# Optimization experiments

Measured on AMD Instinct MI355X. Metric: run time of the kernel, lower is better.

## Reference

```python
import jax, jax.numpy as jnp
import numpy as np

TINY = 1e-9
S, V, H, W = 2, 4, 1024, 1024
PATCH, SKIP = 2, 2
C = PATCH * SKIP
PIX_PER_VIEW = 4096
NP_COARSE = PIX_PER_VIEW // (PATCH * PATCH)   # top-k on coarse grid
N_SAMPLED = NP_COARSE * PATCH * PATCH         # total fine pixels per view
ON_MASK = 0.9
AT_CENTER = 0.8
HC, WC = H // C, W // C


def setup_inputs() -> dict:
    key = jax.random.key(0)
    k1, k2, k3, k4, k5 = jax.random.split(key, 5)
    ys, xs = jnp.meshgrid(jnp.arange(H, dtype=jnp.float32),
                          jnp.arange(W, dtype=jnp.float32), indexing='ij')
    uv1 = jnp.stack([xs.reshape(-1), ys.reshape(-1)])            # (2, H*W): X then Y
    uv = jnp.broadcast_to(uv1[None, None], (S, V, 2, H * W)) + 0.0
    base = jnp.array([[1111.0, 0.0, W / 2.0, 0.0],
                      [0.0, 1111.0, H / 2.0, 0.0],
                      [0.0, 0.0, 1.0, 0.0],
                      [0.0, 0.0, 0.0, 1.0]], dtype=jnp.float32)
    intrinsics = jnp.broadcast_to(base[None], (S, 4, 4)) + 0.0
    A = jax.random.normal(k2, (S, V, 3, 3), dtype=jnp.float32)
    Q, _ = jnp.linalg.qr(A)                                       # random rotations
    t = 2.0 * jax.random.normal(k3, (S, V, 3), dtype=jnp.float32)
    ext = jnp.zeros((S, V, 4, 4), dtype=jnp.float32)
    ext = ext.at[..., :3, :3].set(Q).at[..., :3, 3].set(t).at[..., 3, 3].set(1.0)
    alpha = jax.random.normal(k4, (S, V, H, W), dtype=jnp.float32)
    size = jnp.stack([jnp.full((S, V), H, jnp.int32),
                      jnp.full((S, V), W, jnp.int32)], axis=-1)
    gumbel_u = jax.random.uniform(k5, (S, V, HC * WC), dtype=jnp.float32)
    full_index = jax.random.randint(k1, (S, V), 0, SKIP * SKIP)
    return dict(uv=uv, intrinsics=intrinsics, extrinsics=ext, alpha=alpha,
                size=size, gumbel_u=gumbel_u, full_index=full_index)


def _sample_pixels(uv, alpha, gumbel_u, full_index):
    # mask from alpha, restricted to image center (sampling_at_center=0.8)
    mask = (alpha > 0).astype(jnp.float32)                        # (S,V,H,W)
    r = (1.0 - AT_CENTER) / 2.0
    rh, rw = int(H * r), int(W * r)
    row_ok = (jnp.arange(H) >= rh) & (jnp.arange(H) < H - rh)
    col_ok = (jnp.arange(W) >= rw) & (jnp.arange(W) < W - rw)
    mask = mask * (row_ok[:, None] & col_ok[None, :]).astype(jnp.float32)
    probs = mask / (mask.sum() + 1e-8)                            # global normalization as in torch
    probs = ON_MASK * probs + (1.0 - ON_MASK) / (H * W)
    # pool probabilities onto the coarse (patch*skip) grid
    probs_c = probs.reshape(S, V, HC, C, WC, C).sum(axis=(3, 5))  # (S,V,HC,WC)
    logp = jnp.log(probs_c.reshape(S, V, -1) + TINY)
    g = -jnp.log(-jnp.log(gumbel_u + TINY) + TINY)                # gumbel noise
    idx = jax.lax.top_k(logp + g, NP_COARSE)[1]                   # (S,V,NP_COARSE)
    sm = jnp.zeros((S, V, HC * WC), jnp.float32)
    sm = sm.at[jnp.arange(S)[:, None, None], jnp.arange(V)[None, :, None], idx].set(1.0)
    sm = sm.reshape(S, V, HC, WC)
    # expand each coarse cell into a patch x patch block -> (S,V,H//SKIP,W//SKIP)
    sm = jnp.broadcast_to(sm[:, :, :, None, :, None],
                          (S, V, HC, PATCH, WC, PATCH)).reshape(S, V, H // SKIP, W // SKIP)
    # scatter into a random skip-slot per view, then interleave skip grid
    oh = jax.nn.one_hot(full_index, SKIP * SKIP, dtype=jnp.float32)  # (S,V,SKIP*SKIP)
    full = oh[:, :, :, None, None] * sm[:, :, None, :, :]
    sm = full.reshape(S, V, SKIP, SKIP, H // SKIP, W // SKIP)
    sm = sm.transpose(0, 1, 4, 2, 5, 3).reshape(S, V, H, W)
    # row-major gather of sampled pixels (matches torch boolean-mask gather)
    mflat = sm.reshape(S, V, H * W)
    order = jnp.argsort(-mflat, axis=-1)[..., :N_SAMPLED]         # stable: ones in row-major order
    Xs = jnp.take_along_axis(uv[:, :, 0], order, axis=-1).reshape(S, V, 1, -1, PATCH, PATCH)
    Ys = jnp.take_along_axis(uv[:, :, 1], order, axis=-1).reshape(S, V, 1, -1, PATCH, PATCH)
    return jnp.concatenate([Xs, Ys], axis=2)                      # (S,V,2,NPatch,PATCH,PATCH)


def _rays(uv_s, intrinsics, extrinsics):
    fuv = uv_s.reshape(S, V, 2, -1)                               # (S,V,2,N)
    ray_start = extrinsics[:, :, :3, 3]                           # (S,V,3)
    fx = intrinsics[:, 0, 0][:, None, None]
    fy = intrinsics[:, 1, 1][:, None, None]
    cx = intrinsics[:, 0, 2][:, None, None]
    cy = intrinsics[:, 1, 2][:, None, None]
    x = (fuv[:, :, 0] - cx) / fx                                  # z = 1 lift
    y = (fuv[:, :, 1] - cy) / fy
    ones = jnp.ones_like(x)
    cam = jnp.stack([x, y, ones, ones], axis=2)                   # (S,V,4,N) homogeneous
    world = jnp.einsum('svij,svjn->svin', extrinsics, cam)[:, :, :3]
    d = world - ray_start[..., None]
    d = d / jnp.maximum(jnp.linalg.norm(d, axis=2, keepdims=True), 1e-12)
    return ray_start[:, :, None, :], d.transpose(0, 1, 3, 2)      # (S,V,1,3), (S,V,N,3)


def reference(uv, intrinsics, extrinsics, alpha, size, gumbel_u, full_index):
    uv_s = _sample_pixels(uv, alpha, gumbel_u, full_index)
    ray_start, ray_dir = _rays(uv_s, intrinsics, extrinsics)
    return ray_start, ray_dir, uv_s
```

## Files before the change

kernel.cpp:

```cpp
#include <hip/hip_runtime.h>
#include <math.h>

#define S_ 2
#define V_ 4
#define H_ 1024
#define W_ 1024
#define NCELL 65536
#define NSV 8
#define KSEL 1024
#define CROP_LO 102
#define CROP_HI 922

#define NB1 32768
#define NB2 131072
#define HIST_U4 ((NB1 + NB2) * NSV / 4)

#define OFF_SEL   64
#define OFF_SEG1  256
#define OFF_SEG2  4352
#define OFF_CNT   8448
#define OFF_ROW   8448
#define OFF_KEYS  532736
#define OFF_H1    2629888
#define OFF_H2    3678464

static __device__ __forceinline__ unsigned score_key(float score){
  unsigned ub = __float_as_uint(score);
  return (ub & 0x80000000u) ? ~ub : (ub | 0x80000000u);
}

__global__ __launch_bounds__(1024) void k_init(unsigned* __restrict__ ws32){
  int t = threadIdx.x;
  if (t == 0) ws32[0] = 0u;
  ws32[64 + t] = 0u;
  ws32[64 + 1024 + t] = 0u;
}

__global__ __launch_bounds__(256) void k_count(const float* __restrict__ alpha,
                                               unsigned char* __restrict__ cnt,
                                               unsigned* __restrict__ total){
  int g = blockIdx.x * 256 + threadIdx.x;
  int sv = g >> 16;
  int cell = g & (NCELL - 1);
  int hc = cell >> 8;
  int wc = cell & 255;
  const float4* ap = reinterpret_cast<const float4*>(alpha);
  int c = 0;
  int x0 = wc * 4;
#pragma unroll
  for (int dy = 0; dy < 4; ++dy){
    int y = hc * 4 + dy;
    float4 a = ap[(size_t)(sv * H_ + y) * (W_ / 4) + wc];
    if (y >= CROP_LO && y < CROP_HI){
      c += (a.x > 0.0f) & (x0 + 0 >= CROP_LO) & (x0 + 0 < CROP_HI);
      c += (a.y > 0.0f) & (x0 + 1 >= CROP_LO) & (x0 + 1 < CROP_HI);
      c += (a.z > 0.0f) & (x0 + 2 >= CROP_LO) & (x0 + 2 < CROP_HI);
      c += (a.w > 0.0f) & (x0 + 3 >= CROP_LO) & (x0 + 3 < CROP_HI);
    }
  }
  cnt[g] = (unsigned char)c;
  __shared__ unsigned red[256];
  red[threadIdx.x] = (unsigned)c;
  __syncthreads();
  for (int off = 128; off > 0; off >>= 1){
    if (threadIdx.x < off) red[threadIdx.x] += red[threadIdx.x + off];
    __syncthreads();
  }
  if (threadIdx.x == 0) atomicAdd(total, red[0]);
}

__global__ __launch_bounds__(256) void k_score(const unsigned char* __restrict__ cnt,
                                               const float* __restrict__ gum,
                                               const unsigned* __restrict__ total,
                                               unsigned* __restrict__ keys,
                                               uint4* __restrict__ histz){
  int g = blockIdx.x * 256 + threadIdx.x;
  if (g < HIST_U4) histz[g] = make_uint4(0u, 0u, 0u, 0u);
  float T = (float)(*total);
  float denom = __fadd_rn(T, 1e-8f);
  float inv = __fdiv_rn(1.0f, denom);
  const float COFF = (float)((1.0 - 0.9) / (1024.0 * 1024.0));
  float q_on = __fadd_rn(__fmul_rn(0.9f, inv), COFF);
  int k = cnt[g];
  float pc = __fadd_rn(__fmul_rn((float)k, q_on), __fmul_rn((float)(16 - k), COFF));
  float logp = logf(__fadd_rn(pc, 1e-9f));
  float u = gum[g];
  float gl = logf(__fadd_rn(u, 1e-9f));
  float gmb = -logf(__fadd_rn(-gl, 1e-9f));
  keys[g] = score_key(__fadd_rn(logp, gmb));
}

__global__ __launch_bounds__(256) void k_hist1(const unsigned* __restrict__ keys,
                                               unsigned* __restrict__ hist1,
                                               unsigned* __restrict__ segsum1){
  int sv = blockIdx.x >> 5;
  int chunk = blockIdx.x & 31;
  __shared__ unsigned h[NB1 / 2];
  for (int i = threadIdx.x; i < NB1 / 2; i += 256) h[i] = 0u;
  __syncthreads();
  const uint4* kp = reinterpret_cast<const uint4*>(keys + sv * NCELL + chunk * 2048);
#pragma unroll
  for (int i = 0; i < 2; ++i){
    uint4 k4 = kp[threadIdx.x + i * 256];
    unsigned b;
    b = k4.x >> 17; atomicAdd(&h[b >> 1], 1u << ((b & 1u) << 4));
    b = k4.y >> 17; atomicAdd(&h[b >> 1], 1u << ((b & 1u) << 4));
    b = k4.z >> 17; atomicAdd(&h[b >> 1], 1u << ((b & 1u) << 4));
    b = k4.w >> 17; atomicAdd(&h[b >> 1], 1u << ((b & 1u) << 4));
  }
  __syncthreads();
  unsigned* hb = hist1 + sv * NB1;
  for (int i = threadIdx.x; i < NB1 / 2; i += 256){
    unsigned w = h[i];
    unsigned lo = w & 0xFFFFu, hi = w >> 16;
    if (lo) atomicAdd(&hb[2 * i + 0], lo);
    if (hi) atomicAdd(&hb[2 * i + 1], hi);
  }
  if (threadIdx.x < 128){
    unsigned s = 0;
    for (int i = 0; i < 128; ++i){
      unsigned w = h[threadIdx.x * 128 + i];
      s += (w & 0xFFFFu) + (w >> 16);
    }
    if (s) atomicAdd(&segsum1[sv * 128 + threadIdx.x], s);
  }
}

__global__ __launch_bounds__(256) void k_pick1b(const unsigned* __restrict__ hist1,
                                                const unsigned* __restrict__ segsum1,
                                                unsigned* __restrict__ sel){
  const int sv = blockIdx.x;
  const int t = threadIdx.x;
  __shared__ unsigned ss[128];
  __shared__ int swin;
  __shared__ unsigned stgt;
  __shared__ unsigned sh[256];
  if (t < 128) ss[t] = segsum1[sv * 128 + t];
  __syncthreads();
  if (t == 0){
    unsigned target = KSEL, cum = 0;
    for (int s = 127; s >= 0; --s){
      cum += ss[s];
      if (cum >= target){ swin = s; stgt = target - (cum - ss[s]); break; }
    }
  }
  __syncthreads();
  unsigned v = hist1[sv * NB1 + swin * 256 + t];
  sh[t] = v;
  __syncthreads();
  for (int off = 1; off < 256; off <<= 1){
    unsigned y = (t + off < 256) ? sh[t + off] : 0u;
    __syncthreads();
    sh[t] += y;
    __syncthreads();
  }
  unsigned sufAbove = sh[t] - v;
  if (sufAbove < stgt && sh[t] >= stgt){
    sel[sv * 4 + 0] = (unsigned)(swin * 256 + t);
    sel[sv * 4 + 1] = stgt - sufAbove;
  }
}

__global__ __launch_bounds__(256) void k_hist2(const unsigned* __restrict__ keys,
                                               const unsigned* __restrict__ sel,
                                               unsigned* __restrict__ hist2,
                                               unsigned* __restrict__ segsum2){
  int sv = blockIdx.x >> 5;
  int chunk = blockIdx.x & 31;
  unsigned p15 = sel[sv * 4 + 0];
  __shared__ unsigned seg[128];
  if (threadIdx.x < 128) seg[threadIdx.x] = 0u;
  __syncthreads();
  const uint4* kp = reinterpret_cast<const uint4*>(keys + sv * NCELL + chunk * 2048);
  unsigned* hb = hist2 + sv * NB2;
#pragma unroll
  for (int i = 0; i < 2; ++i){
    uint4 k4 = kp[threadIdx.x + i * 256];
    unsigned kk[4] = {k4.x, k4.y, k4.z, k4.w};
#pragma unroll
    for (int q = 0; q < 4; ++q){
      if ((kk[q] >> 17) == p15){
        unsigned low = kk[q] & 0x1FFFFu;
        atomicAdd(&hb[low], 1u);
        atomicAdd(&seg[low >> 10], 1u);
      }
    }
  }
  __syncthreads();
  if (threadIdx.x < 128){
    unsigned s = seg[threadIdx.x];
    if (s) atomicAdd(&segsum2[sv * 128 + threadIdx.x], s);
  }
}

__global__ __launch_bounds__(256) void k_pick2c(const unsigned* __restrict__ hist2,
                                                const unsigned* __restrict__ segsum2,
                                                unsigned* __restrict__ sel){
  const int sv = blockIdx.x;
  const int t = threadIdx.x;
  __shared__ unsigned ss[128];
  __shared__ int swin;
  __shared__ unsigned stgt;
  __shared__ unsigned sh[256];
  if (t < 128) ss[t] = segsum2[sv * 128 + t];
  __syncthreads();
  if (t == 0){
    unsigned target = sel[sv * 4 + 1];
    unsigned cum = 0;
    for (int s = 127; s >= 0; --s){
      cum += ss[s];
      if (cum >= target){ swin = s; stgt = target - (cum - ss[s]); break; }
    }
  }
  __syncthreads();
  const int s = swin;
  const unsigned t2 = stgt;
  uint4 v = reinterpret_cast<const uint4*>(hist2 + sv * NB2 + s * 1024)[t];
  unsigned csum = v.x + v.y + v.z + v.w;
  sh[t] = csum;
  __syncthreads();
  for (int off = 1; off < 256; off <<= 1){
    unsigned y = (t + off < 256) ? sh[t + off] : 0u;
    __syncthreads();
    sh[t] += y;
    __syncthreads();
  }
  unsigned sufAbove = sh[t] - csum;
  if (sufAbove < t2 && sh[t] >= t2){
    unsigned bb[4] = {v.x, v.y, v.z, v.w};
    unsigned cum = sufAbove;
    for (int b = 3; b >= 0; --b){
      cum += bb[b];
      if (cum >= t2){
        sel[sv * 4 + 2] = (sel[sv * 4 + 0] << 17) | (unsigned)(s * 1024 + t * 4 + b);
        sel[sv * 4 + 3] = t2 - (cum - bb[b]);
        break;
      }
    }
  }
}

__global__ __launch_bounds__(256) void k_rowcnt(const unsigned* __restrict__ keys,
                                                const unsigned* __restrict__ sel,
                                                unsigned* __restrict__ rowcnt){
  int gw = blockIdx.x * 4 + (threadIdx.x >> 6);
  int lane = threadIdx.x & 63;
  int sv = gw >> 8;
  int row = gw & 255;
  const unsigned thr = sel[sv * 4 + 2];
  uint4 k4 = *reinterpret_cast<const uint4*>(keys + sv * NCELL + row * 256 + lane * 4);
  unsigned gt = (k4.x > thr) + (k4.y > thr) + (k4.z > thr) + (k4.w > thr);
  unsigned eq = (k4.x == thr) + (k4.y == thr) + (k4.z == thr) + (k4.w == thr);
  unsigned p = (gt << 16) | eq;
#pragma unroll
  for (int off = 1; off < 64; off <<= 1) p += __shfl_xor(p, off, 64);
  if (lane == 0) rowcnt[gw] = p;
}

static __device__ __forceinline__ unsigned block_excl_scan256(unsigned v, unsigned* lds4, int t){
  int lane = t & 63, w = t >> 6;
  unsigned x = v;
#pragma unroll
  for (int off = 1; off < 64; off <<= 1){
    unsigned y = __shfl_up(x, (unsigned)off, 64);
    if (lane >= off) x += y;
  }
  if (lane == 63) lds4[w] = x;
  __syncthreads();
  unsigned base = 0;
  for (int i = 0; i < w; ++i) base += lds4[i];
  __syncthreads();
  return base + x - v;
}

__global__ __launch_bounds__(256) void k_emitray(const unsigned* __restrict__ keys,
                                                 const unsigned* __restrict__ sel,
                                                 const unsigned* __restrict__ rowcnt,
                                                 const int* __restrict__ fidx,
                                                 const float* __restrict__ intr,
                                                 const float* __restrict__ extr,
                                                 float* __restrict__ out){
  const int sv = blockIdx.x >> 6;
  const int t = threadIdx.x;
  __shared__ unsigned lds4[4];
  __shared__ unsigned sM[256], sP[256], sEqb[256];

  const unsigned thr = sel[sv * 4 + 2];
  const unsigned rem = sel[sv * 4 + 3];

  unsigned rc = rowcnt[sv * 256 + t];
  unsigned gt = rc >> 16, eq = rc & 0xFFFFu;
  unsigned eqbase = block_excl_scan256(eq, lds4, t);
  unsigned take_eq = 0;
  if (rem > eqbase){ take_eq = rem - eqbase; if (take_eq > eq) take_eq = eq; }
  unsigned m = gt + take_eq;
  unsigned P = block_excl_scan256(m, lds4, t);
  sM[t] = m; sP[t] = P; sEqb[t] = eqbase;
  __syncthreads();

  const int lane = t & 63;
  const int row = ((blockIdx.x & 63) << 2) + (t >> 6);
  const unsigned rm = sM[row];
  const unsigned rP = sP[row];
  const unsigned reqb = sEqb[row];

  const int s = sv >> 2;
  const float fx = intr[s * 16 + 0];
  const float cx = intr[s * 16 + 2];
  const float fy = intr[s * 16 + 5];
  const float cy = intr[s * 16 + 6];
  const float e00 = extr[sv * 16 + 0], e01 = extr[sv * 16 + 1], e02 = extr[sv * 16 + 2], e03 = extr[sv * 16 + 3];
  const float e10 = extr[sv * 16 + 4], e11 = extr[sv * 16 + 5], e12 = extr[sv * 16 + 6], e13 = extr[sv * 16 + 7];
  const float e20 = extr[sv * 16 + 8], e21 = extr[sv * 16 + 9], e22 = extr[sv * 16 + 10], e23 = extr[sv * 16 + 11];
  if ((blockIdx.x & 63) == 0 && t < 3) out[sv * 3 + t] = extr[sv * 16 + t * 4 + 3];

  const int fi = fidx[sv];
  const int k1 = (fi >> 1) & 1;
  const int k2 = fi & 1;
  float* out_dir = out + S_ * V_ * 3;
  float* out_uvs = out + S_ * V_ * 3 + S_ * V_ * 4096 * 3;

  uint4 k4 = *reinterpret_cast<const uint4*>(keys + sv * NCELL + row * 256 + lane * 4);
  unsigned kk[4] = {k4.x, k4.y, k4.z, k4.w};

  unsigned laneEq = 0;
#pragma unroll
  for (int q = 0; q < 4; ++q) laneEq += (kk[q] == thr);
  unsigned xe = laneEq;
#pragma unroll
  for (int off = 1; off < 64; off <<= 1){
    unsigned y = __shfl_up(xe, (unsigned)off, 64);
    if (lane >= off) xe += y;
  }
  unsigned eqpre = xe - laneEq;

  bool ssel[4];
  unsigned eqr = reqb + eqpre;
  unsigned laneSel = 0;
#pragma unroll
  for (int q = 0; q < 4; ++q){
    bool sq = (kk[q] > thr);
    if (kk[q] == thr){ if (eqr < rem) sq = true; eqr++; }
    ssel[q] = sq;
    laneSel += sq;
  }
  unsigned xs = laneSel;
#pragma unroll
  for (int off = 1; off < 64; off <<= 1){
    unsigned y = __shfl_up(xs, (unsigned)off, 64);
    if (lane >= off) xs += y;
  }
  unsigned jj = xs - laneSel;

  const unsigned baserank = 4u * rP;
#pragma unroll
  for (int q = 0; q < 4; ++q){
    if (!ssel[q]) continue;
    int wc = lane * 4 + q;
    unsigned base = baserank + 2u * jj;
    int y0 = 4 * row + k1;
    int x0 = 4 * wc + k2;
#pragma unroll
    for (int p1 = 0; p1 < 2; ++p1){
#pragma unroll
      for (int p2 = 0; p2 < 2; ++p2){
        unsigned r = base + (unsigned)p1 * 2u * rm + (unsigned)p2;
        float X = (float)(x0 + 2 * p2);
        float Y = (float)(y0 + 2 * p1);
        out_uvs[(sv * 2 + 0) * 4096 + r] = X;
        out_uvs[(sv * 2 + 1) * 4096 + r] = Y;
        float xx = (X - cx) / fx;
        float yy = (Y - cy) / fy;
        float d0 = (e00 * xx + e01 * yy + e02 + e03) - e03;
        float d1 = (e10 * xx + e11 * yy + e12 + e13) - e13;
        float d2 = (e20 * xx + e21 * yy + e22 + e23) - e23;
        float nrm = sqrtf(d0 * d0 + d1 * d1 + d2 * d2);
        float den = fmaxf(nrm, 1e-12f);
        size_t ob = ((size_t)sv * 4096 + r) * 3;
        out_dir[ob + 0] = d0 / den;
        out_dir[ob + 1] = d1 / den;
        out_dir[ob + 2] = d2 / den;
      }
    }
    jj++;
  }
}

extern "C" void kernel_launch(void* const* d_in, const int* in_sizes, int n_in,
                              void* d_out, int out_size, void* d_ws, size_t ws_size,
                              hipStream_t stream){
  (void)in_sizes; (void)n_in; (void)out_size; (void)ws_size;
  const float* intr       = (const float*)d_in[1];
  const float* extr       = (const float*)d_in[2];
  const float* alpha      = (const float*)d_in[3];
  const float* gum        = (const float*)d_in[5];
  const int*   full_index = (const int*)d_in[6];
  float* out = (float*)d_out;

  char* ws = (char*)d_ws;
  unsigned*      ws32    = (unsigned*)ws;
  unsigned*      total   = (unsigned*)ws;
  unsigned*      sel     = (unsigned*)(ws + OFF_SEL);
  unsigned*      segsum1 = (unsigned*)(ws + OFF_SEG1);
  unsigned*      segsum2 = (unsigned*)(ws + OFF_SEG2);
  unsigned char* cnt     = (unsigned char*)(ws + OFF_CNT);
  unsigned*      rowcnt  = (unsigned*)(ws + OFF_ROW);
  unsigned*      keys    = (unsigned*)(ws + OFF_KEYS);
  unsigned*      hist1   = (unsigned*)(ws + OFF_H1);
  unsigned*      hist2   = (unsigned*)(ws + OFF_H2);
  uint4*         histz   = (uint4*)(ws + OFF_H1);

  hipLaunchKernelGGL(k_init,    dim3(1), dim3(1024), 0, stream, ws32);
  hipLaunchKernelGGL(k_count,   dim3(NSV * NCELL / 256), dim3(256), 0, stream, alpha, cnt, total);
  hipLaunchKernelGGL(k_score,   dim3(NSV * NCELL / 256), dim3(256), 0, stream, cnt, gum, total, keys, histz);
  hipLaunchKernelGGL(k_hist1,   dim3(NSV * 32), dim3(256), 0, stream, keys, hist1, segsum1);
  hipLaunchKernelGGL(k_pick1b,  dim3(NSV), dim3(256), 0, stream, hist1, segsum1, sel);
  hipLaunchKernelGGL(k_hist2,   dim3(NSV * 32), dim3(256), 0, stream, keys, sel, hist2, segsum2);
  hipLaunchKernelGGL(k_pick2c,  dim3(NSV), dim3(256), 0, stream, hist2, segsum2, sel);
  hipLaunchKernelGGL(k_rowcnt,  dim3(512), dim3(256), 0, stream, keys, sel, rowcnt);
  hipLaunchKernelGGL(k_emitray, dim3(512), dim3(256), 0, stream, keys, sel, rowcnt, full_index, intr, extr, out);
}
```

Baseline: 82.48 us.

## Fuse score, histogram and pick stages using last-block completion counters

Removes the init kernel and folds workspace zeroing into the count kernel. The global atomic total becomes per-block partial sums that each scoring block reduces itself. Scoring is fused with the first radix histogram, and each pick step now runs in the last block to finish (detected with done counters and threadfences), so the launch count drops from nine to five. In exchange every scoring block re-reduces 2048 partials, and the pick work now runs serially inside a single tail block.

```diff
diff --git a/kernel.cpp b/kernel.cpp
--- a/kernel.cpp
+++ b/kernel.cpp
@@ -16,30 +16,30 @@
 #define HIST_U4 ((NB1 + NB2) * NSV / 4)
 
 #define OFF_SEL   64
+#define OFF_DONE  192
 #define OFF_SEG1  256
 #define OFF_SEG2  4352
-#define OFF_CNT   8448
-#define OFF_ROW   8448
-#define OFF_KEYS  532736
-#define OFF_H1    2629888
-#define OFF_H2    3678464
+#define OFF_PART  8448
+#define OFF_CNT   16640
+#define OFF_ROW   16640
+#define OFF_KEYS  540928
+#define OFF_H1    2638080
+#define OFF_H2    3686656
 
 static __device__ __forceinline__ unsigned score_key(float score){
   unsigned ub = __float_as_uint(score);
   return (ub & 0x80000000u) ? ~ub : (ub | 0x80000000u);
 }
 
-__global__ __launch_bounds__(1024) void k_init(unsigned* __restrict__ ws32){
-  int t = threadIdx.x;
-  if (t == 0) ws32[0] = 0u;
-  ws32[64 + t] = 0u;
-  ws32[64 + 1024 + t] = 0u;
-}
-
 __global__ __launch_bounds__(256) void k_count(const float* __restrict__ alpha,
                                                unsigned char* __restrict__ cnt,
-                                               unsigned* __restrict__ total){
+                                               unsigned* __restrict__ partial,
+                                               uint4* __restrict__ histz,
+                                               unsigned* __restrict__ ws32){
   int g = blockIdx.x * 256 + threadIdx.x;
+  if (g < HIST_U4) histz[g] = make_uint4(0u, 0u, 0u, 0u);
+  if (g < 2048) ws32[64 + g] = 0u;
+  if (g < 16)   ws32[48 + g] = 0u;
   int sv = g >> 16;
   int cell = g & (NCELL - 1);
   int hc = cell >> 8;
@@ -66,116 +66,138 @@
     if (threadIdx.x < off) red[threadIdx.x] += red[threadIdx.x + off];
     __syncthreads();
   }
-  if (threadIdx.x == 0) atomicAdd(total, red[0]);
-}
-
-__global__ __launch_bounds__(256) void k_score(const unsigned char* __restrict__ cnt,
-                                               const float* __restrict__ gum,
-                                               const unsigned* __restrict__ total,
-                                               unsigned* __restrict__ keys,
-                                               uint4* __restrict__ histz){
-  int g = blockIdx.x * 256 + threadIdx.x;
-  if (g < HIST_U4) histz[g] = make_uint4(0u, 0u, 0u, 0u);
-  float T = (float)(*total);
+  if (threadIdx.x == 0) partial[blockIdx.x] = red[0];
+}
+
+__global__ __launch_bounds__(256) void k_scoreh(const unsigned char* __restrict__ cnt,
+                                                const float* __restrict__ gum,
+                                                const unsigned* __restrict__ partial,
+                                                unsigned* __restrict__ keys,
+                                                unsigned* __restrict__ hist1,
+                                                unsigned* __restrict__ segsum1,
+                                                unsigned* __restrict__ done1,
+                                                unsigned* __restrict__ sel){
+  const int sv = blockIdx.x >> 5;
+  const int chunk = blockIdx.x & 31;
+  const int t = threadIdx.x;
+  __shared__ unsigned h[NB1 / 2];
+  __shared__ unsigned red[256];
+  __shared__ unsigned ss[128];
+  __shared__ unsigned sh2[256];
+  __shared__ int swin;
+  __shared__ unsigned stgt;
+  __shared__ int slast;
+
+  unsigned psum = 0;
+#pragma unroll
+  for (int j = 0; j < 8; ++j) psum += partial[t + j * 256];
+  red[t] = psum;
+  __syncthreads();
+  for (int off = 128; off > 0; off >>= 1){
+    if (t < off) red[t] += red[t + off];
+    __syncthreads();
+  }
+  const float T = (float)red[0];
+
   float denom = __fadd_rn(T, 1e-8f);
   float inv = __fdiv_rn(1.0f, denom);
   const float COFF = (float)((1.0 - 0.9) / (1024.0 * 1024.0));
   float q_on = __fadd_rn(__fmul_rn(0.9f, inv), COFF);
-  int k = cnt[g];
-  float pc = __fadd_rn(__fmul_rn((float)k, q_on), __fmul_rn((float)(16 - k), COFF));
-  float logp = logf(__fadd_rn(pc, 1e-9f));
-  float u = gum[g];
-  float gl = logf(__fadd_rn(u, 1e-9f));
-  float gmb = -logf(__fadd_rn(-gl, 1e-9f));
-  keys[g] = score_key(__fadd_rn(logp, gmb));
-}
-
-__global__ __launch_bounds__(256) void k_hist1(const unsigned* __restrict__ keys,
-                                               unsigned* __restrict__ hist1,
-                                               unsigned* __restrict__ segsum1){
-  int sv = blockIdx.x >> 5;
-  int chunk = blockIdx.x & 31;
-  __shared__ unsigned h[NB1 / 2];
-  for (int i = threadIdx.x; i < NB1 / 2; i += 256) h[i] = 0u;
-  __syncthreads();
-  const uint4* kp = reinterpret_cast<const uint4*>(keys + sv * NCELL + chunk * 2048);
-#pragma unroll
-  for (int i = 0; i < 2; ++i){
-    uint4 k4 = kp[threadIdx.x + i * 256];
-    unsigned b;
-    b = k4.x >> 17; atomicAdd(&h[b >> 1], 1u << ((b & 1u) << 4));
-    b = k4.y >> 17; atomicAdd(&h[b >> 1], 1u << ((b & 1u) << 4));
-    b = k4.z >> 17; atomicAdd(&h[b >> 1], 1u << ((b & 1u) << 4));
-    b = k4.w >> 17; atomicAdd(&h[b >> 1], 1u << ((b & 1u) << 4));
+
+  unsigned kreg[8];
+  const int base = sv * NCELL + chunk * 2048;
+#pragma unroll
+  for (int i = 0; i < 8; ++i){
+    int g = base + i * 256 + t;
+    int k = cnt[g];
+    float pc = __fadd_rn(__fmul_rn((float)k, q_on), __fmul_rn((float)(16 - k), COFF));
+    float logp = logf(__fadd_rn(pc, 1e-9f));
+    float u = gum[g];
+    float gl = logf(__fadd_rn(u, 1e-9f));
+    float gmb = -logf(__fadd_rn(-gl, 1e-9f));
+    kreg[i] = score_key(__fadd_rn(logp, gmb));
+    keys[g] = kreg[i];
+  }
+
+  for (int i = t; i < NB1 / 2; i += 256) h[i] = 0u;
+  __syncthreads();
+#pragma unroll
+  for (int i = 0; i < 8; ++i){
+    unsigned b = kreg[i] >> 17;
+    atomicAdd(&h[b >> 1], 1u << ((b & 1u) << 4));
   }
   __syncthreads();
   unsigned* hb = hist1 + sv * NB1;
-  for (int i = threadIdx.x; i < NB1 / 2; i += 256){
+  for (int i = t; i < NB1 / 2; i += 256){
     unsigned w = h[i];
     unsigned lo = w & 0xFFFFu, hi = w >> 16;
     if (lo) atomicAdd(&hb[2 * i + 0], lo);
     if (hi) atomicAdd(&hb[2 * i + 1], hi);
   }
-  if (threadIdx.x < 128){
+  if (t < 128){
     unsigned s = 0;
     for (int i = 0; i < 128; ++i){
-      unsigned w = h[threadIdx.x * 128 + i];
+      unsigned w = h[t * 128 + i];
       s += (w & 0xFFFFu) + (w >> 16);
     }
-    if (s) atomicAdd(&segsum1[sv * 128 + threadIdx.x], s);
-  }
-}
-
-__global__ __launch_bounds__(256) void k_pick1b(const unsigned* __restrict__ hist1,
-                                                const unsigned* __restrict__ segsum1,
-                                                unsigned* __restrict__ sel){
-  const int sv = blockIdx.x;
+    if (s) atomicAdd(&segsum1[sv * 128 + t], s);
+  }
+
+  __threadfence();
+  if (t == 0) slast = (atomicAdd(&done1[sv], 1u) == 31u) ? 1 : 0;
+  __syncthreads();
+  if (slast){
+    __threadfence();
+    if (t < 128) ss[t] = segsum1[sv * 128 + t];
+    __syncthreads();
+    if (t == 0){
+      unsigned target = KSEL, cum = 0;
+      for (int s = 127; s >= 0; --s){
+        cum += ss[s];
+        if (cum >= target){ swin = s; stgt = target - (cum - ss[s]); break; }
+      }
+    }
+    __syncthreads();
+    unsigned v = hist1[sv * NB1 + swin * 256 + t];
+    sh2[t] = v;
+    __syncthreads();
+    for (int off = 1; off < 256; off <<= 1){
+      unsigned y = (t + off < 256) ? sh2[t + off] : 0u;
+      __syncthreads();
+      sh2[t] += y;
+      __syncthreads();
+    }
+    unsigned sufAbove = sh2[t] - v;
+    if (sufAbove < stgt && sh2[t] >= stgt){
+      sel[sv * 4 + 0] = (unsigned)(swin * 256 + t);
+      sel[sv * 4 + 1] = stgt - sufAbove;
+    }
+  }
+}
+
+__global__ __launch_bounds__(256) void k_hist2p(const unsigned* __restrict__ keys,
+                                                unsigned* __restrict__ sel,
+                                                unsigned* __restrict__ hist2,
+                                                unsigned* __restrict__ segsum2,
+                                                unsigned* __restrict__ done2){
+  const int sv = blockIdx.x >> 5;
+  const int chunk = blockIdx.x & 31;
   const int t = threadIdx.x;
+  __shared__ unsigned seg[128];
   __shared__ unsigned ss[128];
+  __shared__ unsigned sh2[256];
   __shared__ int swin;
   __shared__ unsigned stgt;
-  __shared__ unsigned sh[256];
-  if (t < 128) ss[t] = segsum1[sv * 128 + t];
-  __syncthreads();
-  if (t == 0){
-    unsigned target = KSEL, cum = 0;
-    for (int s = 127; s >= 0; --s){
-      cum += ss[s];
-      if (cum >= target){ swin = s; stgt = target - (cum - ss[s]); break; }
-    }
-  }
-  __syncthreads();
-  unsigned v = hist1[sv * NB1 + swin * 256 + t];
-  sh[t] = v;
-  __syncthreads();
-  for (int off = 1; off < 256; off <<= 1){
-    unsigned y = (t + off < 256) ? sh[t + off] : 0u;
-    __syncthreads();
-    sh[t] += y;
-    __syncthreads();
-  }
-  unsigned sufAbove = sh[t] - v;
-  if (sufAbove < stgt && sh[t] >= stgt){
-    sel[sv * 4 + 0] = (unsigned)(swin * 256 + t);
-    sel[sv * 4 + 1] = stgt - sufAbove;
-  }
-}
-
-__global__ __launch_bounds__(256) void k_hist2(const unsigned* __restrict__ keys,
-                                               const unsigned* __restrict__ sel,
-                                               unsigned* __restrict__ hist2,
-                                               unsigned* __restrict__ segsum2){
-  int sv = blockIdx.x >> 5;
-  int chunk = blockIdx.x & 31;
+  __shared__ int slast;
+
   unsigned p15 = sel[sv * 4 + 0];
-  __shared__ unsigned seg[128];
-  if (threadIdx.x < 128) seg[threadIdx.x] = 0u;
+  if (t < 128) seg[t] = 0u;
   __syncthreads();
   const uint4* kp = reinterpret_cast<const uint4*>(keys + sv * NCELL + chunk * 2048);
   unsigned* hb = hist2 + sv * NB2;
 #pragma unroll
   for (int i = 0; i < 2; ++i){
-    uint4 k4 = kp[threadIdx.x + i * 256];
+    uint4 k4 = kp[t + i * 256];
     unsigned kk[4] = {k4.x, k4.y, k4.z, k4.w};
 #pragma unroll
     for (int q = 0; q < 4; ++q){
@@ -187,54 +209,50 @@
     }
   }
   __syncthreads();
-  if (threadIdx.x < 128){
-    unsigned s = seg[threadIdx.x];
-    if (s) atomicAdd(&segsum2[sv * 128 + threadIdx.x], s);
-  }
-}
-
-__global__ __launch_bounds__(256) void k_pick2c(const unsigned* __restrict__ hist2,
-                                                const unsigned* __restrict__ segsum2,
-                                                unsigned* __restrict__ sel){
-  const int sv = blockIdx.x;
-  const int t = threadIdx.x;
-  __shared__ unsigned ss[128];
-  __shared__ int swin;
-  __shared__ unsigned stgt;
-  __shared__ unsigned sh[256];
-  if (t < 128) ss[t] = segsum2[sv * 128 + t];
-  __syncthreads();
-  if (t == 0){
-    unsigned target = sel[sv * 4 + 1];
-    unsigned cum = 0;
-    for (int s = 127; s >= 0; --s){
-      cum += ss[s];
-      if (cum >= target){ swin = s; stgt = target - (cum - ss[s]); break; }
-    }
-  }
-  __syncthreads();
-  const int s = swin;
-  const unsigned t2 = stgt;
-  uint4 v = reinterpret_cast<const uint4*>(hist2 + sv * NB2 + s * 1024)[t];
-  unsigned csum = v.x + v.y + v.z + v.w;
-  sh[t] = csum;
-  __syncthreads();
-  for (int off = 1; off < 256; off <<= 1){
-    unsigned y = (t + off < 256) ? sh[t + off] : 0u;
-    __syncthreads();
-    sh[t] += y;
-    __syncthreads();
-  }
-  unsigned sufAbove = sh[t] - csum;
-  if (sufAbove < t2 && sh[t] >= t2){
-    unsigned bb[4] = {v.x, v.y, v.z, v.w};
-    unsigned cum = sufAbove;
-    for (int b = 3; b >= 0; --b){
-      cum += bb[b];
-      if (cum >= t2){
-        sel[sv * 4 + 2] = (sel[sv * 4 + 0] << 17) | (unsigned)(s * 1024 + t * 4 + b);
-        sel[sv * 4 + 3] = t2 - (cum - bb[b]);
-        break;
+  if (t < 128){
+    unsigned s = seg[t];
+    if (s) atomicAdd(&segsum2[sv * 128 + t], s);
+  }
+
+  __threadfence();
+  if (t == 0) slast = (atomicAdd(&done2[sv], 1u) == 31u) ? 1 : 0;
+  __syncthreads();
+  if (slast){
+    __threadfence();
+    if (t < 128) ss[t] = segsum2[sv * 128 + t];
+    __syncthreads();
+    if (t == 0){
+      unsigned target = sel[sv * 4 + 1];
+      unsigned cum = 0;
+      for (int s = 127; s >= 0; --s){
+        cum += ss[s];
+        if (cum >= target){ swin = s; stgt = target - (cum - ss[s]); break; }
+      }
+    }
+    __syncthreads();
+    const int s = swin;
+    const unsigned t2 = stgt;
+    uint4 v = reinterpret_cast<const uint4*>(hist2 + sv * NB2 + s * 1024)[t];
+    unsigned csum = v.x + v.y + v.z + v.w;
+    sh2[t] = csum;
+    __syncthreads();
+    for (int off = 1; off < 256; off <<= 1){
+      unsigned y = (t + off < 256) ? sh2[t + off] : 0u;
+      __syncthreads();
+      sh2[t] += y;
+      __syncthreads();
+    }
+    unsigned sufAbove = sh2[t] - csum;
+    if (sufAbove < t2 && sh2[t] >= t2){
+      unsigned bb[4] = {v.x, v.y, v.z, v.w};
+      unsigned cum = sufAbove;
+      for (int b = 3; b >= 0; --b){
+        cum += bb[b];
+        if (cum >= t2){
+          sel[sv * 4 + 2] = (sel[sv * 4 + 0] << 17) | (unsigned)(s * 1024 + t * 4 + b);
+          sel[sv * 4 + 3] = t2 - (cum - bb[b]);
+          break;
+        }
       }
     }
   }
@@ -399,10 +417,12 @@
 
   char* ws = (char*)d_ws;
   unsigned*      ws32    = (unsigned*)ws;
-  unsigned*      total   = (unsigned*)ws;
   unsigned*      sel     = (unsigned*)(ws + OFF_SEL);
+  unsigned*      done1   = (unsigned*)(ws + OFF_DONE);
+  unsigned*      done2   = (unsigned*)(ws + OFF_DONE + 32);
   unsigned*      segsum1 = (unsigned*)(ws + OFF_SEG1);
   unsigned*      segsum2 = (unsigned*)(ws + OFF_SEG2);
+  unsigned*      partial = (unsigned*)(ws + OFF_PART);
   unsigned char* cnt     = (unsigned char*)(ws + OFF_CNT);
   unsigned*      rowcnt  = (unsigned*)(ws + OFF_ROW);
   unsigned*      keys    = (unsigned*)(ws + OFF_KEYS);
@@ -410,13 +430,9 @@
   unsigned*      hist2   = (unsigned*)(ws + OFF_H2);
   uint4*         histz   = (uint4*)(ws + OFF_H1);
 
-  hipLaunchKernelGGL(k_init,    dim3(1), dim3(1024), 0, stream, ws32);
-  hipLaunchKernelGGL(k_count,   dim3(NSV * NCELL / 256), dim3(256), 0, stream, alpha, cnt, total);
-  hipLaunchKernelGGL(k_score,   dim3(NSV * NCELL / 256), dim3(256), 0, stream, cnt, gum, total, keys, histz);
-  hipLaunchKernelGGL(k_hist1,   dim3(NSV * 32), dim3(256), 0, stream, keys, hist1, segsum1);
-  hipLaunchKernelGGL(k_pick1b,  dim3(NSV), dim3(256), 0, stream, hist1, segsum1, sel);
-  hipLaunchKernelGGL(k_hist2,   dim3(NSV * 32), dim3(256), 0, stream, keys, sel, hist2, segsum2);
-  hipLaunchKernelGGL(k_pick2c,  dim3(NSV), dim3(256), 0, stream, hist2, segsum2, sel);
+  hipLaunchKernelGGL(k_count,   dim3(NSV * NCELL / 256), dim3(256), 0, stream, alpha, cnt, partial, histz, ws32);
+  hipLaunchKernelGGL(k_scoreh,  dim3(256), dim3(256), 0, stream, cnt, gum, partial, keys, hist1, segsum1, done1, sel);
+  hipLaunchKernelGGL(k_hist2p,  dim3(256), dim3(256), 0, stream, keys, sel, hist2, segsum2, done2);
   hipLaunchKernelGGL(k_rowcnt,  dim3(512), dim3(256), 0, stream, keys, sel, rowcnt);
   hipLaunchKernelGGL(k_emitray, dim3(512), dim3(256), 0, stream, keys, sel, rowcnt, full_index, intr, extr, out);
 }
```

Result: slower. 84.57 us (+2.5%).
